# Kernel optimization log

Hardware: AMD Instinct MI355X
Metric: run time of the kernel (lower is better)

Reference implementation:

```python
import jax, jax.numpy as jnp
import numpy as np

DIM = 2048
HEADS = 16
B = 2
T = 2048


def setup_inputs() -> dict:
    key = jax.random.key(0)
    k_x, k_qkv, k_out, k_b = jax.random.split(key, 4)
    inv = DIM ** -0.5
    return {
        "x": jax.random.normal(k_x, (B, T, DIM), dtype=jnp.float32),
        "w_qkv": jax.random.normal(k_qkv, (DIM, 3 * DIM), dtype=jnp.float32) * inv,
        "w_out": jax.random.normal(k_out, (DIM, DIM), dtype=jnp.float32) * inv,
        "b_out": jnp.zeros((DIM,), dtype=jnp.float32),
    }


def reference(x, w_qkv, w_out, b_out):
    b, t, e = x.shape
    h = HEADS
    d = e // h
    scale = d ** -0.5
    qkv = x @ w_qkv                              # [b, t, 3e]
    q, k, v = jnp.split(qkv, 3, axis=-1)
    # [b, t, e] -> [b, h, t, d]
    q, k, v = (a.reshape(b, t, h, d).transpose(0, 2, 1, 3) for a in (q, k, v))
    dots = jnp.einsum("bhid,bhjd->bhij", q, k) * scale  # [b, h, t, t]
    causal_mask = jnp.triu(jnp.ones((t, t), dtype=bool), k=1)  # True where j > i
    dots = jnp.where(causal_mask[None, None, :, :], -jnp.inf, dots)
    attn = jax.nn.softmax(dots, axis=-1)
    out = jnp.einsum("bhij,bhjd->bhid", attn, v)  # [b, h, t, d]
    out = out.transpose(0, 2, 1, 3).reshape(b, t, e)
    return out @ w_out + b_out
```

## Files before the change

### kernel.cpp

```cpp
#include <hip/hip_runtime.h>
#include <stdint.h>

#define BATCH 2
#define TDIM 2048
#define EDIM 2048
#define NH 16
#define HD 128
#define E3 6144
#define MROWS 4096
#define QKS 4096

typedef short v8bf __attribute__((ext_vector_type(8)));
typedef float v4f  __attribute__((ext_vector_type(4)));

typedef __attribute__((address_space(3))) uint8_t lds_u8;
typedef __attribute__((address_space(1))) uint8_t glb_u8;

__device__ __forceinline__ void gload16(const void* g, void* l) {
    __builtin_amdgcn_global_load_lds((const glb_u8*)g, (lds_u8*)l, 16, 0, 0);
}

__device__ __forceinline__ ushort f2bf(float f) {
    uint32_t u = __float_as_uint(f);
    return (ushort)((u + 0x7fffu + ((u >> 16) & 1u)) >> 16);
}

__device__ __forceinline__ void tcvt_body(const float* __restrict__ in, ushort* __restrict__ out,
                                          int R, int C, int tcb, int trb, int tid) {
    __shared__ float t[32][33];
    const int tc = tcb * 32, tr = trb * 32;
    const int row = tid >> 3, c4 = (tid & 7) * 4;
    const float4 v = *reinterpret_cast<const float4*>(in + (size_t)(tr + row) * C + tc + c4);
    t[row][c4] = v.x; t[row][c4 + 1] = v.y; t[row][c4 + 2] = v.z; t[row][c4 + 3] = v.w;
    __syncthreads();
    const int oc = tid >> 3, r4 = (tid & 7) * 4;
    ushort4 o = make_ushort4(f2bf(t[r4][oc]), f2bf(t[r4 + 1][oc]),
                             f2bf(t[r4 + 2][oc]), f2bf(t[r4 + 3][oc]));
    *reinterpret_cast<ushort4*>(out + (size_t)(tc + oc) * R + tr + r4) = o;
}

#define NB_T1 12288
#define NB_T2 4096
#define NB_CV 2048

__global__ void prep_kernel(const float* __restrict__ x, const float* __restrict__ w_qkv,
                            const float* __restrict__ w_out, ushort* __restrict__ xb,
                            ushort* __restrict__ wqkvT, ushort* __restrict__ woutT) {
    const int bid = blockIdx.x;
    const int tid = threadIdx.x;
    if (bid < NB_T1) {
        tcvt_body(w_qkv, wqkvT, EDIM, E3, bid % (E3 / 32), bid / (E3 / 32), tid);
    } else if (bid < NB_T1 + NB_T2) {
        const int b2 = bid - NB_T1;
        tcvt_body(w_out, woutT, EDIM, EDIM, b2 % (EDIM / 32), b2 / (EDIM / 32), tid);
    } else {
        const int b3 = bid - NB_T1 - NB_T2;
        int i = (b3 * 256 + tid) * 4;
        const int stride = NB_CV * 256 * 4;
        const int n = MROWS * EDIM;
        for (; i < n; i += stride) {
            const float4 v = *reinterpret_cast<const float4*>(x + i);
            ushort4 o = make_ushort4(f2bf(v.x), f2bf(v.y), f2bf(v.z), f2bf(v.w));
            *reinterpret_cast<ushort4*>(xb + i) = o;
        }
    }
}

template <int MODE>
__global__ void gemm_kernel(const ushort* __restrict__ A, const ushort* __restrict__ Bt,
                            void* __restrict__ Cv, const float* __restrict__ bias,
                            ushort* __restrict__ vtout,
                            int Mdim, int Ndim, int Kdim) {
    __shared__ __align__(16) ushort As[128 * 64];
    __shared__ __align__(16) ushort Bs[128 * 64];
    const int tid = threadIdx.x;
    const int lane = tid & 63;
    const int wv = tid >> 6;
    const int l4 = lane >> 4, l16 = lane & 15;
    const int nbn = Ndim >> 7;
    const int nwg = (Mdim >> 7) * nbn;
    int bid = blockIdx.x;
    bid = (bid & 7) * (nwg >> 3) + (bid >> 3);
    const int bm = bid / nbn, bn = bid % nbn;
    const int wr = wv >> 1, wc = wv & 1;

    const ushort* Abase = A + (size_t)(bm * 128) * Kdim;
    const ushort* Bbase = Bt + (size_t)(bn * 128) * Kdim;

    v4f acc[4][4] = {};

    for (int k0 = 0; k0 < Kdim; k0 += 64) {
#pragma unroll
        for (int i = 0; i < 4; ++i) {
            const int c = i * 256 + tid;
            const int row = c >> 3;
            const int kc = (c & 7) ^ (row & 7);
            gload16(Abase + (size_t)row * Kdim + k0 + kc * 8, &As[(i * 256 + wv * 64) * 8]);
        }
#pragma unroll
        for (int i = 0; i < 4; ++i) {
            const int c = i * 256 + tid;
            const int row = c >> 3;
            const int kc = (c & 7) ^ (row & 7);
            gload16(Bbase + (size_t)row * Kdim + k0 + kc * 8, &Bs[(i * 256 + wv * 64) * 8]);
        }
        __syncthreads();
#pragma unroll
        for (int kk = 0; kk < 2; ++kk) {
            v8bf af[4], bfr[4];
#pragma unroll
            for (int m = 0; m < 4; ++m) {
                const int r = wr * 64 + m * 16 + l16;
                const int slot = (kk * 4 + l4) ^ (r & 7);
                af[m] = *reinterpret_cast<const v8bf*>(&As[r * 64 + slot * 8]);
            }
#pragma unroll
            for (int n = 0; n < 4; ++n) {
                const int r = wc * 64 + n * 16 + l16;
                const int slot = (kk * 4 + l4) ^ (r & 7);
                bfr[n] = *reinterpret_cast<const v8bf*>(&Bs[r * 64 + slot * 8]);
            }
#pragma unroll
            for (int m = 0; m < 4; ++m)
#pragma unroll
                for (int n = 0; n < 4; ++n)
                    acc[m][n] = __builtin_amdgcn_mfma_f32_16x16x32_bf16(af[m], bfr[n], acc[m][n], 0, 0, 0);
        }
        __syncthreads();
    }

    const int r0 = bm * 128 + wr * 64 + l4 * 4;
    const int c0 = bn * 128 + wc * 64 + l16;
    if (MODE == 1) {
        float* Cf = (float*)Cv;
#pragma unroll
        for (int n = 0; n < 4; ++n) {
            const float bv = bias[c0 + n * 16];
#pragma unroll
            for (int m = 0; m < 4; ++m)
#pragma unroll
                for (int j = 0; j < 4; ++j)
                    Cf[(size_t)(r0 + m * 16 + j) * Ndim + c0 + n * 16] = acc[m][n][j] + bv;
        }
    } else if (MODE == 2 && bn >= 32) {
        const int h = bn - 32;
#pragma unroll
        for (int m = 0; m < 4; ++m) {
            const int r = r0 + m * 16;
            const int b = r >> 11, t0 = r & 2047;
#pragma unroll
            for (int n = 0; n < 4; ++n) {
                const int dcol = wc * 64 + n * 16 + l16;
                ushort* vp = vtout + (size_t)((b * 16 + h) * 128 + dcol) * TDIM + t0;
#pragma unroll
                for (int j = 0; j < 4; ++j)
                    vp[j] = f2bf(acc[m][n][j]);
            }
        }
    } else {
        const int cstride = (MODE == 2) ? QKS : Ndim;
        ushort* Cb = (ushort*)Cv;
#pragma unroll
        for (int n = 0; n < 4; ++n)
#pragma unroll
            for (int m = 0; m < 4; ++m)
#pragma unroll
                for (int j = 0; j < 4; ++j)
                    Cb[(size_t)(r0 + m * 16 + j) * cstride + c0 + n * 16] = f2bf(acc[m][n][j]);
    }
}

__global__ __launch_bounds__(256, 2) void flash_kernel(const ushort* __restrict__ qk,
                                                       const ushort* __restrict__ vt,
                                                       ushort* __restrict__ ao) {
    __shared__ __align__(16) ushort Kl[2][64 * 128];
    __shared__ __align__(16) ushort Vl[2][128 * 64];
    __shared__ __align__(16) ushort Pl[128 * 64];

    const int xi = blockIdx.x;
    const int ti = (xi & 1) ? (xi >> 1) : (15 - (xi >> 1));
    const int h = blockIdx.y;
    const int b = blockIdx.z;
    const int tid = threadIdx.x;
    const int lane = tid & 63;
    const int wv = tid >> 6;
    const int l4 = lane >> 4, l16 = lane & 15;

    const int rbs[2]  = {ti * 64 + wv * 16, TDIM - 64 * (ti + 1) + wv * 16};
    const int diag[2] = {ti, 31 - ti};
    const int nkt = 32 - ti;

    v8bf qf[2][4];
#pragma unroll
    for (int mg = 0; mg < 2; ++mg) {
        const ushort* qp = qk + (size_t)(b * TDIM + rbs[mg] + l16) * QKS + h * HD + l4 * 8;
#pragma unroll
        for (int d0 = 0; d0 < 4; ++d0) {
            v8bf r = *reinterpret_cast<const v8bf*>(qp + d0 * 32);
            v8bf o;
#pragma unroll
            for (int e = 0; e < 8; ++e) {
                const float f = __uint_as_float(((uint32_t)(ushort)r[e]) << 16) * 0.08838834764831845f;
                o[e] = (short)f2bf(f);
            }
            qf[mg][d0] = o;
        }
    }

    float mrun[2][4], lrun[2][4];
#pragma unroll
    for (int mg = 0; mg < 2; ++mg)
#pragma unroll
        for (int j = 0; j < 4; ++j) { mrun[mg][j] = -1e30f; lrun[mg][j] = 0.0f; }
    v4f oacc[2][8] = {};

    const ushort* kbase = qk + (size_t)(b * TDIM) * QKS + EDIM + h * HD;
    const ushort* vbase = vt + (size_t)((b * 16 + h) * HD) * TDIM;

#define STAGE(BUF, KT)                                                                        \
    do {                                                                                      \
        _Pragma("unroll") for (int i = 0; i < 4; ++i) {                                       \
            const int c = i * 256 + tid;                                                      \
            const int row = c >> 4;                                                           \
            const int dc = (c & 15) ^ (row & 7);                                              \
            gload16(kbase + (size_t)((KT) * 64 + row) * QKS + dc * 8,                         \
                    &Kl[BUF][(i * 256 + wv * 64) * 8]);                                       \
        }                                                                                     \
        _Pragma("unroll") for (int i = 0; i < 4; ++i) {                                       \
            const int c = i * 256 + tid;                                                      \
            const int row = c >> 3;                                                           \
            const int jc = (c & 7) ^ (row & 7);                                               \
            gload16(vbase + (size_t)row * TDIM + (KT) * 64 + jc * 8,                          \
                    &Vl[BUF][(i * 256 + wv * 64) * 8]);                                       \
        }                                                                                     \
    } while (0)

    STAGE(0, 0);
    __syncthreads();
    int cur = 0;

    for (int kt = 0; kt < nkt; ++kt) {
        if (kt + 1 < nkt) STAGE(cur ^ 1, kt + 1);

        const bool act0 = (kt <= diag[0]);
        const ushort* Kb = &Kl[cur][0];
        const ushort* Vb = &Vl[cur][0];

        v4f s[2][4] = {};
#pragma unroll
        for (int d0 = 0; d0 < 4; ++d0) {
            v8bf kf[4];
#pragma unroll
            for (int kvn = 0; kvn < 4; ++kvn) {
                const int r = kvn * 16 + l16;
                const int slot = (d0 * 4 + l4) ^ (r & 7);
                kf[kvn] = *reinterpret_cast<const v8bf*>(&Kb[r * 128 + slot * 8]);
            }
#pragma unroll
            for (int kvn = 0; kvn < 4; ++kvn) {
                if (act0)
                    s[0][kvn] = __builtin_amdgcn_mfma_f32_16x16x32_bf16(qf[0][d0], kf[kvn], s[0][kvn], 0, 0, 0);
                s[1][kvn] = __builtin_amdgcn_mfma_f32_16x16x32_bf16(qf[1][d0], kf[kvn], s[1][kvn], 0, 0, 0);
            }
        }

#pragma unroll
        for (int mg = 0; mg < 2; ++mg) {
            if (mg == 0 && !act0) continue;

            float sv[4][4];
#pragma unroll
            for (int kvn = 0; kvn < 4; ++kvn)
#pragma unroll
                for (int j = 0; j < 4; ++j)
                    sv[kvn][j] = s[mg][kvn][j];

            if (kt == diag[mg]) {
                const int rg = rbs[mg] + l4 * 4;
#pragma unroll
                for (int kvn = 0; kvn < 4; ++kvn) {
                    const int cg = kt * 64 + kvn * 16 + l16;
#pragma unroll
                    for (int j = 0; j < 4; ++j)
                        if (cg > rg + j) sv[kvn][j] = -__builtin_inff();
                }
            }

            float pm[4], dmax = -1e30f;
#pragma unroll
            for (int j = 0; j < 4; ++j) {
                float m0 = fmaxf(fmaxf(sv[0][j], sv[1][j]), fmaxf(sv[2][j], sv[3][j]));
                m0 = fmaxf(m0, __shfl_xor(m0, 1));
                m0 = fmaxf(m0, __shfl_xor(m0, 2));
                m0 = fmaxf(m0, __shfl_xor(m0, 4));
                m0 = fmaxf(m0, __shfl_xor(m0, 8));
                pm[j] = m0;
                dmax = fmaxf(dmax, m0 - mrun[mg][j]);
            }
            if (!__all(dmax <= 8.0f)) {
                float corr[4];
#pragma unroll
                for (int j = 0; j < 4; ++j) {
                    const float mn = fmaxf(mrun[mg][j], pm[j]);
                    corr[j] = __expf(mrun[mg][j] - mn);
                    mrun[mg][j] = mn;
                    lrun[mg][j] *= corr[j];
                }
#pragma unroll
                for (int n = 0; n < 8; ++n)
#pragma unroll
                    for (int j = 0; j < 4; ++j)
                        oacc[mg][n][j] *= corr[j];
            }

            float p[4][4];
#pragma unroll
            for (int kvn = 0; kvn < 4; ++kvn)
#pragma unroll
                for (int j = 0; j < 4; ++j)
                    p[kvn][j] = __expf(sv[kvn][j] - mrun[mg][j]);
#pragma unroll
            for (int j = 0; j < 4; ++j)
                lrun[mg][j] += p[0][j] + p[1][j] + p[2][j] + p[3][j];

            const int row = wv * 32 + mg * 16 + l4 * 4;
#pragma unroll
            for (int kvn = 0; kvn < 4; ++kvn) {
                const int cc = kvn * 2 + (l16 >> 3);
#pragma unroll
                for (int j = 0; j < 4; ++j) {
                    const int r = row + j;
                    Pl[r * 64 + ((cc ^ (r & 7)) * 8) + (l16 & 7)] = f2bf(p[kvn][j]);
                }
            }
        }

#pragma unroll
        for (int kk = 0; kk < 2; ++kk) {
            v8bf pf[2];
#pragma unroll
            for (int mg = 0; mg < 2; ++mg) {
                if (mg == 0 && !act0) continue;
                const int r = wv * 32 + mg * 16 + l16;
                const int slot = (kk * 4 + l4) ^ (r & 7);
                pf[mg] = *reinterpret_cast<const v8bf*>(&Pl[r * 64 + slot * 8]);
            }
#pragma unroll
            for (int n = 0; n < 8; ++n) {
                const int dr = n * 16 + l16;
                const int slot = (kk * 4 + l4) ^ (dr & 7);
                v8bf vf = *reinterpret_cast<const v8bf*>(&Vb[dr * 64 + slot * 8]);
                if (act0)
                    oacc[0][n] = __builtin_amdgcn_mfma_f32_16x16x32_bf16(pf[0], vf, oacc[0][n], 0, 0, 0);
                oacc[1][n] = __builtin_amdgcn_mfma_f32_16x16x32_bf16(pf[1], vf, oacc[1][n], 0, 0, 0);
            }
        }
        __syncthreads();
        cur ^= 1;
    }
#undef STAGE

#pragma unroll
    for (int mg = 0; mg < 2; ++mg) {
        float inv[4];
#pragma unroll
        for (int j = 0; j < 4; ++j) {
            float l = lrun[mg][j];
            l += __shfl_xor(l, 1);
            l += __shfl_xor(l, 2);
            l += __shfl_xor(l, 4);
            l += __shfl_xor(l, 8);
            inv[j] = 1.0f / l;
        }
        ushort* aop = ao + (size_t)(b * TDIM + rbs[mg] + l4 * 4) * EDIM + h * HD + l16;
#pragma unroll
        for (int n = 0; n < 8; ++n)
#pragma unroll
            for (int j = 0; j < 4; ++j)
                aop[(size_t)j * EDIM + n * 16] = f2bf(oacc[mg][n][j] * inv[j]);
    }
}

extern "C" void kernel_launch(void* const* d_in, const int* in_sizes, int n_in,
                              void* d_out, int out_size, void* d_ws, size_t ws_size,
                              hipStream_t stream) {
    (void)in_sizes; (void)n_in; (void)out_size; (void)ws_size;
    const float* x     = (const float*)d_in[0];
    const float* w_qkv = (const float*)d_in[1];
    const float* w_out = (const float*)d_in[2];
    const float* b_out = (const float*)d_in[3];

    uint8_t* ws = (uint8_t*)d_ws;
    ushort* qk    = (ushort*)(ws);
    ushort* vtb   = (ushort*)(ws + 33554432u);
    ushort* woutT = (ushort*)(ws + 50331648u);
    ushort* xb    = (ushort*)(ws + 58720256u);
    ushort* wqkvT = (ushort*)(ws + 75497472u);
    ushort* ao    = wqkvT;

    prep_kernel<<<NB_T1 + NB_T2 + NB_CV, 256, 0, stream>>>(x, w_qkv, w_out, xb, wqkvT, woutT);

    gemm_kernel<2><<<(MROWS / 128) * (E3 / 128), 256, 0, stream>>>(
        xb, wqkvT, (void*)qk, nullptr, vtb, MROWS, E3, EDIM);

    flash_kernel<<<dim3(16, NH, BATCH), 256, 0, stream>>>(qk, vtb, ao);

    gemm_kernel<1><<<(MROWS / 128) * (EDIM / 128), 256, 0, stream>>>(
        ao, woutT, d_out, b_out, nullptr, MROWS, EDIM, EDIM);
}
```

Baseline: 256.4 us.

## Replace QKV projection GEMM with 256x256-tile double-buffered 8-wave kernel

Adds a new QKV projection GEMM that uses 256x256 output tiles, 512 threads (8 waves) and double-buffered LDS staging. Global-to-LDS loads for the next K tile are interleaved with quadrant-wise MFMA phases under explicit barriers and setprio. The larger tile raises data reuse per loaded byte and the pipelining is meant to hide global load latency. In exchange it uses about 128KB of LDS, allowing one block per CU, and launches only 384 workgroups, which may leave some CUs underused on the final wave.

```diff
diff --git a/kernel.cpp b/kernel.cpp
--- a/kernel.cpp
+++ b/kernel.cpp
@@ -66,10 +66,156 @@
     }
 }
 
-template <int MODE>
+__global__ __launch_bounds__(512, 1) void gemm256q_kernel(const ushort* __restrict__ A,
+                                                          const ushort* __restrict__ Bt,
+                                                          ushort* __restrict__ qkout,
+                                                          ushort* __restrict__ vtout,
+                                                          int Mdim, int Ndim, int Kdim) {
+    __shared__ __align__(16) ushort AL[2][2][128 * 64];
+    __shared__ __align__(16) ushort BL[2][2][128 * 64];
+    const int tid = threadIdx.x;
+    const int lane = tid & 63;
+    const int wv = tid >> 6;
+    const int l4 = lane >> 4, l16 = lane & 15;
+    const int wr = wv >> 2, wc = wv & 3;
+    const int nbn = Ndim >> 8;
+    const int nwg = (Mdim >> 8) * nbn;
+    int bid = blockIdx.x;
+    bid = (bid & 7) * (nwg >> 3) + (bid >> 3);
+    const int bm = bid / nbn, bn = bid % nbn;
+
+    const ushort* Abase = A + (size_t)(bm * 256) * Kdim;
+    const ushort* Bbase = Bt + (size_t)(bn * 256) * Kdim;
+    const int NT = Kdim >> 6;
+
+#define STG_HALF(LDST, GB, H, T)                                                              \
+    do {                                                                                      \
+        { const int s = wv * 64 + lane; const int row = s >> 3;                               \
+          const int kc = (s & 7) ^ (row & 7);                                                 \
+          gload16(GB + (size_t)((H) * 128 + row) * Kdim + (T) * 64 + kc * 8,                  \
+                  &LDST[(wv * 64) * 8]); }                                                    \
+        { const int s = 512 + wv * 64 + lane; const int row = s >> 3;                         \
+          const int kc = (s & 7) ^ (row & 7);                                                 \
+          gload16(GB + (size_t)((H) * 128 + row) * Kdim + (T) * 64 + kc * 8,                  \
+                  &LDST[(512 + wv * 64) * 8]); }                                              \
+    } while (0)
+#define STG_A(BUF, T) do { STG_HALF(AL[BUF][0], Abase, 0, T); STG_HALF(AL[BUF][1], Abase, 1, T); } while (0)
+#define STG_B(BUF, T) do { STG_HALF(BL[BUF][0], Bbase, 0, T); STG_HALF(BL[BUF][1], Bbase, 1, T); } while (0)
+
+#define LOAD_AF(BUF, MQ)                                                                      \
+    _Pragma("unroll") for (int m = 0; m < 4; ++m)                                             \
+    _Pragma("unroll") for (int kk = 0; kk < 2; ++kk) {                                        \
+        const int rl = (MQ) * 64 + m * 16 + l16;                                              \
+        const int slot = (kk * 4 + l4) ^ (l16 & 7);                                           \
+        af[m][kk] = *reinterpret_cast<const v8bf*>(&AL[BUF][wr][rl * 64 + slot * 8]);         \
+    }
+#define LOAD_BF(BUF, NQ)                                                                      \
+    _Pragma("unroll") for (int n = 0; n < 2; ++n)                                             \
+    _Pragma("unroll") for (int kk = 0; kk < 2; ++kk) {                                        \
+        const int rl = (wc & 1) * 64 + (NQ) * 32 + n * 16 + l16;                              \
+        const int slot = (kk * 4 + l4) ^ (l16 & 7);                                           \
+        bf[n][kk] = *reinterpret_cast<const v8bf*>(&BL[BUF][wc >> 1][rl * 64 + slot * 8]);    \
+    }
+#define MFMA16(MQ, NQ)                                                                        \
+    __builtin_amdgcn_s_setprio(1);                                                            \
+    _Pragma("unroll") for (int kk = 0; kk < 2; ++kk)                                          \
+    _Pragma("unroll") for (int m = 0; m < 4; ++m)                                             \
+    _Pragma("unroll") for (int n = 0; n < 2; ++n)                                             \
+        acc[MQ][m][NQ][n] = __builtin_amdgcn_mfma_f32_16x16x32_bf16(                          \
+            af[m][kk], bf[n][kk], acc[MQ][m][NQ][n], 0, 0, 0);                                \
+    __builtin_amdgcn_s_setprio(0);
+#define BARS() __builtin_amdgcn_s_barrier(); __builtin_amdgcn_sched_barrier(0)
+#define WAITLGKM() asm volatile("s_waitcnt lgkmcnt(0)" ::: "memory"); __builtin_amdgcn_sched_barrier(0)
+#define WAITVM0() asm volatile("s_waitcnt vmcnt(0)" ::: "memory")
+
+    v4f acc[2][4][2][2] = {};
+
+    STG_A(0, 0); STG_B(0, 0);
+    WAITVM0();
+    BARS();
+
+    for (int T = 0; T < NT; T += 2) {
+        v8bf af[4][2], bf[2][2];
+        LOAD_AF(0, 0) LOAD_BF(0, 0)
+        STG_A(1, T + 1);
+        BARS(); WAITLGKM();
+        MFMA16(0, 0)
+        BARS();
+        LOAD_BF(0, 1)
+        STG_B(1, T + 1);
+        BARS(); WAITLGKM();
+        MFMA16(0, 1)
+        BARS();
+        LOAD_AF(0, 1) LOAD_BF(0, 0)
+        BARS(); WAITLGKM();
+        MFMA16(1, 0)
+        BARS();
+        LOAD_BF(0, 1)
+        BARS(); WAITLGKM();
+        MFMA16(1, 1)
+        WAITVM0();
+        BARS();
+        LOAD_AF(1, 0) LOAD_BF(1, 0)
+        if (T + 2 < NT) STG_A(0, T + 2);
+        BARS(); WAITLGKM();
+        MFMA16(0, 0)
+        BARS();
+        LOAD_BF(1, 1)
+        if (T + 2 < NT) STG_B(0, T + 2);
+        BARS(); WAITLGKM();
+        MFMA16(0, 1)
+        BARS();
+        LOAD_AF(1, 1) LOAD_BF(1, 0)
+        BARS(); WAITLGKM();
+        MFMA16(1, 0)
+        BARS();
+        LOAD_BF(1, 1)
+        BARS(); WAITLGKM();
+        MFMA16(1, 1)
+        WAITVM0();
+        BARS();
+    }
+#undef STG_HALF
+#undef STG_A
+#undef STG_B
+#undef LOAD_AF
+#undef LOAD_BF
+#undef MFMA16
+#undef BARS
+#undef WAITLGKM
+#undef WAITVM0
+
+    const bool isV = (bn >= 16);
+#pragma unroll
+    for (int mq = 0; mq < 2; ++mq)
+#pragma unroll
+        for (int m = 0; m < 4; ++m) {
+            const int r = bm * 256 + wr * 128 + mq * 64 + m * 16 + l4 * 4;
+#pragma unroll
+            for (int nq = 0; nq < 2; ++nq)
+#pragma unroll
+                for (int n = 0; n < 2; ++n) {
+                    const int c = bn * 256 + wc * 64 + nq * 32 + n * 16 + l16;
+                    if (isV) {
+                        const int cv = c - 4096;
+                        const int h = cv >> 7, d = cv & 127;
+                        const int b = r >> 11, t0 = r & 2047;
+                        ushort* vp = vtout + (size_t)(((b << 4) + h) * 128 + d) * TDIM + t0;
+#pragma unroll
+                        for (int j = 0; j < 4; ++j)
+                            vp[j] = f2bf(acc[mq][m][nq][n][j]);
+                    } else {
+#pragma unroll
+                        for (int j = 0; j < 4; ++j)
+                            qkout[(size_t)(r + j) * QKS + c] = f2bf(acc[mq][m][nq][n][j]);
+                    }
+                }
+        }
+}
+
+template <int OUTF32>
 __global__ void gemm_kernel(const ushort* __restrict__ A, const ushort* __restrict__ Bt,
                             void* __restrict__ Cv, const float* __restrict__ bias,
-                            ushort* __restrict__ vtout,
                             int Mdim, int Ndim, int Kdim) {
     __shared__ __align__(16) ushort As[128 * 64];
     __shared__ __align__(16) ushort Bs[128 * 64];
@@ -131,7 +277,7 @@
 
     const int r0 = bm * 128 + wr * 64 + l4 * 4;
     const int c0 = bn * 128 + wc * 64 + l16;
-    if (MODE == 1) {
+    if (OUTF32) {
         float* Cf = (float*)Cv;
 #pragma unroll
         for (int n = 0; n < 4; ++n) {
@@ -142,31 +288,15 @@
                 for (int j = 0; j < 4; ++j)
                     Cf[(size_t)(r0 + m * 16 + j) * Ndim + c0 + n * 16] = acc[m][n][j] + bv;
         }
-    } else if (MODE == 2 && bn >= 32) {
-        const int h = bn - 32;
-#pragma unroll
-        for (int m = 0; m < 4; ++m) {
-            const int r = r0 + m * 16;
-            const int b = r >> 11, t0 = r & 2047;
-#pragma unroll
-            for (int n = 0; n < 4; ++n) {
-                const int dcol = wc * 64 + n * 16 + l16;
-                ushort* vp = vtout + (size_t)((b * 16 + h) * 128 + dcol) * TDIM + t0;
+    } else {
+        ushort* Cb = (ushort*)Cv;
+#pragma unroll
+        for (int n = 0; n < 4; ++n)
+#pragma unroll
+            for (int m = 0; m < 4; ++m)
 #pragma unroll
                 for (int j = 0; j < 4; ++j)
-                    vp[j] = f2bf(acc[m][n][j]);
-            }
-        }
-    } else {
-        const int cstride = (MODE == 2) ? QKS : Ndim;
-        ushort* Cb = (ushort*)Cv;
-#pragma unroll
-        for (int n = 0; n < 4; ++n)
-#pragma unroll
-            for (int m = 0; m < 4; ++m)
-#pragma unroll
-                for (int j = 0; j < 4; ++j)
-                    Cb[(size_t)(r0 + m * 16 + j) * cstride + c0 + n * 16] = f2bf(acc[m][n][j]);
+                    Cb[(size_t)(r0 + m * 16 + j) * Ndim + c0 + n * 16] = f2bf(acc[m][n][j]);
     }
 }
 
@@ -400,11 +530,11 @@
 
     prep_kernel<<<NB_T1 + NB_T2 + NB_CV, 256, 0, stream>>>(x, w_qkv, w_out, xb, wqkvT, woutT);
 
-    gemm_kernel<2><<<(MROWS / 128) * (E3 / 128), 256, 0, stream>>>(
-        xb, wqkvT, (void*)qk, nullptr, vtb, MROWS, E3, EDIM);
+    gemm256q_kernel<<<(MROWS / 256) * (E3 / 256), 512, 0, stream>>>(
+        xb, wqkvT, qk, vtb, MROWS, E3, EDIM);
 
     flash_kernel<<<dim3(16, NH, BATCH), 256, 0, stream>>>(qk, vtb, ao);
 
     gemm_kernel<1><<<(MROWS / 128) * (EDIM / 128), 256, 0, stream>>>(
-        ao, woutT, d_out, b_out, nullptr, MROWS, EDIM, EDIM);
-}
+        ao, woutT, d_out, b_out, MROWS, EDIM, EDIM);
+}
```

Result: slower. 278.5 us (+8.6%).
